# Performance work log

Measured on AMD Instinct MI355X. Metric: run time of the kernel, lower is better.

## Reference

```python
import jax, jax.numpy as jnp
import numpy as np

S_INDEX, E_INDEX = 3, 5
S = 26
C = 80
IMG_SIZE = 416.0
LAMBDA_COORD = 5.0
LAMBDA_NOOBJ = 0.5
YOLO_STEP = 3
N = YOLO_STEP * (5 + C)  # 255
ANCHOR = jnp.array([[10, 13], [16, 30], [33, 23], [30, 61], [62, 45],
                    [59, 119], [116, 90], [156, 198], [373, 326]], dtype=jnp.float32)
B, NB = 256, 32


def setup_inputs() -> dict:
    key = jax.random.key(0)
    k1, k2, k3, k4, k5 = jax.random.split(key, 5)
    batch_x = jax.random.normal(k1, (B, N, S, S), dtype=jnp.float32)
    cls = jax.random.randint(k2, (B, NB), 0, C).astype(jnp.float32)
    cxy = jax.random.uniform(k3, (B, NB, 2), minval=0.0, maxval=IMG_SIZE - 1e-3)
    wh = jax.random.uniform(k4, (B, NB, 2), minval=5.0, maxval=IMG_SIZE / 2)
    batch_box = jnp.concatenate([cls[..., None], cxy, wh], axis=-1)  # [B, NB, 5]
    batch_index = jax.random.randint(k5, (B, NB), S_INDEX, E_INDEX + 1)  # anchors of this scale
    return {"batch_x": batch_x, "batch_box": batch_box, "batch_index": batch_index}


def _iou(b1, b2):
    # torch IOU with +1 area convention and negative values clipped to 0
    A = (b1[:, 2] - b1[:, 0] + 1) * (b1[:, 3] - b1[:, 1] + 1)
    Bt = (b2[:, 2] - b2[:, 0] + 1) * (b2[:, 3] - b2[:, 1] + 1)
    CM = ((jnp.minimum(b1[:, 2], b2[:, 2]) - jnp.maximum(b1[:, 0], b2[:, 0]) + 1) *
          (jnp.minimum(b1[:, 3], b2[:, 3]) - jnp.maximum(b1[:, 1], b2[:, 1]) + 1))
    r = CM / (A + Bt - CM)
    return jnp.where(r < 0, 0.0, r)


def _image_loss(x, box, n_index):
    # x: [N, S, S], box: [nb, 5] = (class, cx, cy, w, h), n_index: [nb] global anchor ids
    nb = box.shape[0]
    div = IMG_SIZE / S
    now_index = n_index - S_INDEX            # local anchor id in {0,1,2}
    base = now_index * (5 + C)               # channel offset per box
    ix = (box[:, 1] / div).astype(jnp.int32)
    iy = (box[:, 2] / div).astype(jnp.int32)
    ax = (box[:, 1] - ix.astype(x.dtype) * div) / div
    ay = (box[:, 2] - iy.astype(x.dtype) * div) / div
    now_x = x[:, ix, iy]                     # [N, nb] gather of responsible cells
    it = jnp.arange(nb)
    obj_pred = now_x[base, it]
    rax = now_x[base + 1, it]
    ray = now_x[base + 2, it]
    rw = ANCHOR[n_index, 0] * jnp.exp(4.0 * jax.nn.sigmoid(now_x[base + 3, it]) - 2.0)
    rh = ANCHOR[n_index, 1] * jnp.exp(4.0 * jax.nn.sigmoid(now_x[base + 4, it]) - 2.0)
    b1 = jnp.stack([rax * div - rw / 2, ray * div - rh / 2,
                    rax * div + rw / 2, ray * div + rh / 2], axis=1)
    b2 = jnp.stack([ax * div - box[:, 3] / 2, ay * div - box[:, 4] / 2,
                    ax * div + box[:, 3] / 2, ay * div + box[:, 4] / 2], axis=1)
    iou = _iou(b1, b2)
    hot = jax.nn.one_hot(box[:, 0].astype(jnp.int32), C, dtype=x.dtype)
    lbl_idx = base[:, None] + 5 + jnp.arange(C)[None, :]   # [nb, C]
    label = now_x[lbl_idx, it[:, None]]                     # [nb, C]
    mse = lambda a, b: jnp.mean((a - b) ** 2)
    loss = LAMBDA_COORD * mse(obj_pred, iou)
    loss = loss + mse(label, hot)
    loss = loss + LAMBDA_COORD * mse(rax, ax)
    loss = loss + LAMBDA_COORD * mse(ray, ay)
    loss = loss + LAMBDA_COORD * mse(rw / IMG_SIZE, box[:, 3] / IMG_SIZE)
    loss = loss + LAMBDA_COORD * mse(rh / IMG_SIZE, box[:, 4] / IMG_SIZE)
    # no-object loss over the 3 objectness channels, minus responsible cells
    mask = jnp.zeros((N, S, S), dtype=bool)
    mask = mask.at[jnp.array([0, 5 + C, 2 * (5 + C)])].set(True)
    mask = mask.at[base, ix, iy].set(False)
    cnt = jnp.sum(mask).astype(x.dtype)
    noobj = jnp.sum(jnp.where(mask, x, 0.0) ** 2) / cnt
    return loss + LAMBDA_NOOBJ * noobj


def reference(batch_x, batch_box, batch_index):
    losses = jax.vmap(_image_loss)(batch_x, batch_box, batch_index)  # [B]
    return jnp.sum(losses).reshape(1)
```

## Files before the change

### kernel.cpp

```cpp
#include <hip/hip_runtime.h>

#define S_DIM 26
#define NCLS 80
#define CELLS 676
#define NB 32
#define NCH 255
#define NPLANE 2028
#define CH_BLK 85

__global__ __launch_bounds__(256)
void yolo_loss_kernel(const float* __restrict__ x,
                      const float* __restrict__ box,
                      const int*   __restrict__ nidx,
                      float* __restrict__ out)
{
    const int b   = blockIdx.x;
    const int tid = threadIdx.x;
    const float* xb = x + (size_t)b * (NCH * CELLS);

    __shared__ int   s_key[NB];
    __shared__ int   s_off[NB];
    __shared__ int   s_cls[NB];
    __shared__ float s_obj2[NB];
    __shared__ float s_part[4][4];

    float accA = 0.f;
    float accL = 0.f;
    float accP = 0.f;
    float accD = 0.f;
    float accC = 0.f;

    if (tid < NB) {
        const float* bx = box + ((size_t)b * NB + tid) * 5;
        float cls = bx[0], cx = bx[1], cy = bx[2], w = bx[3], h = bx[4];
        int n  = nidx[b * NB + tid];
        int ni = n - 3;
        int ix = (int)(cx * (1.0f / 16.0f));
        int iy = (int)(cy * (1.0f / 16.0f));
        float ax = (cx - (float)ix * 16.0f) * (1.0f / 16.0f);
        float ay = (cy - (float)iy * 16.0f) * (1.0f / 16.0f);
        int cell = ix * S_DIM + iy;
        int off  = ni * CH_BLK * CELLS + cell;

        s_key[tid] = ni * CELLS + cell;
        s_off[tid] = off;
        s_cls[tid] = (int)cls;

        float obj = xb[off];
        float rax = xb[off + 1 * CELLS];
        float ray = xb[off + 2 * CELLS];
        float t3  = xb[off + 3 * CELLS];
        float t4  = xb[off + 4 * CELLS];
        s_obj2[tid] = obj * obj;

        const float AW[3] = {30.f, 62.f, 59.f};
        const float AH[3] = {61.f, 45.f, 119.f};
        float sig3 = 1.0f / (1.0f + expf(-t3));
        float sig4 = 1.0f / (1.0f + expf(-t4));
        float rw = AW[ni] * expf(4.0f * sig3 - 2.0f);
        float rh = AH[ni] * expf(4.0f * sig4 - 2.0f);

        float b1x0 = rax * 16.f - rw * 0.5f, b1y0 = ray * 16.f - rh * 0.5f;
        float b1x1 = rax * 16.f + rw * 0.5f, b1y1 = ray * 16.f + rh * 0.5f;
        float b2x0 = ax * 16.f - w * 0.5f,   b2y0 = ay * 16.f - h * 0.5f;
        float b2x1 = ax * 16.f + w * 0.5f,   b2y1 = ay * 16.f + h * 0.5f;
        float A  = (rw + 1.f) * (rh + 1.f);
        float Bt = (w + 1.f) * (h + 1.f);
        float CM = (fminf(b1x1, b2x1) - fmaxf(b1x0, b2x0) + 1.f) *
                   (fminf(b1y1, b2y1) - fmaxf(b1y0, b2y0) + 1.f);
        float r = CM / (A + Bt - CM);
        float iou = (r < 0.f) ? 0.f : r;

        float d;
        d = obj - iou;                  accA += d * d;
        d = rax - ax;                   accA += d * d;
        d = ray - ay;                   accA += d * d;
        d = (rw - w) * (1.f / 416.f);   accA += d * d;
        d = (rh - h) * (1.f / 416.f);   accA += d * d;
    }
    __syncthreads();

    if (tid < NB) {
        int key = s_key[tid];
        bool first = true;
        for (int s = 0; s < tid; ++s)
            if (s_key[s] == key) { first = false; break; }
        if (first) { accC += 1.0f; accD += s_obj2[tid]; }
    }

    for (int u = tid; u < NB * NCLS; u += 256) {
        int t = u / NCLS;
        int c = u - t * NCLS;
        float val = xb[s_off[t] + (5 + c) * CELLS];
        float hot = (c == s_cls[t]) ? 1.0f : 0.0f;
        float d = val - hot;
        accL += d * d;
    }

    for (int u = tid; u < NPLANE; u += 256) {
        int pl   = u / CELLS;
        int cell = u - pl * CELLS;
        float v = xb[pl * CH_BLK * CELLS + cell];
        accP += v * v;
    }

    float v1 = accA * (5.0f / 32.0f) + accL * (1.0f / 2560.0f);
    float v2 = accP;
    float v3 = accD;
    float v4 = accC;
    #pragma unroll
    for (int o = 32; o > 0; o >>= 1) {
        v1 += __shfl_down(v1, o, 64);
        v2 += __shfl_down(v2, o, 64);
        v3 += __shfl_down(v3, o, 64);
        v4 += __shfl_down(v4, o, 64);
    }
    int wave = tid >> 6;
    if ((tid & 63) == 0) {
        s_part[0][wave] = v1; s_part[1][wave] = v2;
        s_part[2][wave] = v3; s_part[3][wave] = v4;
    }
    __syncthreads();
    if (tid == 0) {
        float t1 = s_part[0][0] + s_part[0][1] + s_part[0][2] + s_part[0][3];
        float t2 = s_part[1][0] + s_part[1][1] + s_part[1][2] + s_part[1][3];
        float t3 = s_part[2][0] + s_part[2][1] + s_part[2][2] + s_part[2][3];
        float t4 = s_part[3][0] + s_part[3][1] + s_part[3][2] + s_part[3][3];
        float cnt  = 2028.0f - t4;
        float loss = t1 + 0.5f * (t2 - t3) / cnt;
        atomicAdd(out, loss);
    }
}

extern "C" void kernel_launch(void* const* d_in, const int* in_sizes, int n_in,
                              void* d_out, int out_size, void* d_ws, size_t ws_size,
                              hipStream_t stream) {
    const float* x    = (const float*)d_in[0];
    const float* box  = (const float*)d_in[1];
    const int*   nidx = (const int*)d_in[2];
    float* out = (float*)d_out;

    hipMemsetAsync(out, 0, sizeof(float) * out_size, stream);
    yolo_loss_kernel<<<dim3(256), dim3(256), 0, stream>>>(x, box, nidx, out);
}
```

Before: 228.0 us.

## Split per-image loss across three blocks and vectorize objectness plane reads

Launches three blocks per image instead of one. One block sums squared values over the three objectness planes using float4 loads. The other two each handle 16 boxes' head and class terms, and each contributes its partial loss through an atomicAdd. The aim is more parallelism across the GPU and fewer serialized loads per block. The cost is three times as many atomics, repeated metadata setup, and an unused unscaled kernel variant left in the file.

```diff
diff --git a/kernel.cpp b/kernel.cpp
--- a/kernel.cpp
+++ b/kernel.cpp
@@ -5,8 +5,47 @@
 #define CELLS 676
 #define NB 32
 #define NCH 255
-#define NPLANE 2028
 #define CH_BLK 85
+#define PLANE_F4 507
+#define F4_PER_PLANE 169
+#define F4_PLANE_STRIDE 14365
+
+__device__ inline float head_terms(const float* __restrict__ xb,
+                                   int off, int ni,
+                                   float w, float h, float ax, float ay)
+{
+    float obj = xb[off];
+    float rax = xb[off + 1 * CELLS];
+    float ray = xb[off + 2 * CELLS];
+    float t3  = xb[off + 3 * CELLS];
+    float t4  = xb[off + 4 * CELLS];
+
+    const float AW[3] = {30.f, 62.f, 59.f};
+    const float AH[3] = {61.f, 45.f, 119.f};
+    float sig3 = 1.0f / (1.0f + expf(-t3));
+    float sig4 = 1.0f / (1.0f + expf(-t4));
+    float rw = AW[ni] * expf(4.0f * sig3 - 2.0f);
+    float rh = AH[ni] * expf(4.0f * sig4 - 2.0f);
+
+    float b1x0 = rax * 16.f - rw * 0.5f, b1y0 = ray * 16.f - rh * 0.5f;
+    float b1x1 = rax * 16.f + rw * 0.5f, b1y1 = ray * 16.f + rh * 0.5f;
+    float b2x0 = ax * 16.f - w * 0.5f,   b2y0 = ay * 16.f - h * 0.5f;
+    float b2x1 = ax * 16.f + w * 0.5f,   b2y1 = ay * 16.f + h * 0.5f;
+    float A  = (rw + 1.f) * (rh + 1.f);
+    float Bt = (w + 1.f) * (h + 1.f);
+    float CM = (fminf(b1x1, b2x1) - fmaxf(b1x0, b2x0) + 1.f) *
+               (fminf(b1y1, b2y1) - fmaxf(b1y0, b2y0) + 1.f);
+    float r = CM / (A + Bt - CM);
+    float iou = (r < 0.f) ? 0.f : r;
+
+    float acc = 0.f, d;
+    d = obj - iou;                  acc += d * d;
+    d = rax - ax;                   acc += d * d;
+    d = ray - ay;                   acc += d * d;
+    d = (rw - w) * (1.f / 416.f);   acc += d * d;
+    d = (rh - h) * (1.f / 416.f);   acc += d * d;
+    return acc;
+}
 
 __global__ __launch_bounds__(256)
 void yolo_loss_kernel(const float* __restrict__ x,
@@ -14,121 +53,217 @@
                       const int*   __restrict__ nidx,
                       float* __restrict__ out)
 {
-    const int b   = blockIdx.x;
-    const int tid = threadIdx.x;
+    const int b     = blockIdx.x;
+    const int slice = blockIdx.y;
+    const int tid   = threadIdx.x;
     const float* xb = x + (size_t)b * (NCH * CELLS);
 
     __shared__ int   s_key[NB];
     __shared__ int   s_off[NB];
     __shared__ int   s_cls[NB];
     __shared__ float s_obj2[NB];
-    __shared__ float s_part[4][4];
-
-    float accA = 0.f;
-    float accL = 0.f;
-    float accP = 0.f;
-    float accD = 0.f;
-    float accC = 0.f;
-
-    if (tid < NB) {
-        const float* bx = box + ((size_t)b * NB + tid) * 5;
-        float cls = bx[0], cx = bx[1], cy = bx[2], w = bx[3], h = bx[4];
-        int n  = nidx[b * NB + tid];
-        int ni = n - 3;
-        int ix = (int)(cx * (1.0f / 16.0f));
-        int iy = (int)(cy * (1.0f / 16.0f));
-        float ax = (cx - (float)ix * 16.0f) * (1.0f / 16.0f);
-        float ay = (cy - (float)iy * 16.0f) * (1.0f / 16.0f);
-        int cell = ix * S_DIM + iy;
-        int off  = ni * CH_BLK * CELLS + cell;
-
-        s_key[tid] = ni * CELLS + cell;
-        s_off[tid] = off;
-        s_cls[tid] = (int)cls;
-
-        float obj = xb[off];
-        float rax = xb[off + 1 * CELLS];
-        float ray = xb[off + 2 * CELLS];
-        float t3  = xb[off + 3 * CELLS];
-        float t4  = xb[off + 4 * CELLS];
-        s_obj2[tid] = obj * obj;
-
-        const float AW[3] = {30.f, 62.f, 59.f};
-        const float AH[3] = {61.f, 45.f, 119.f};
-        float sig3 = 1.0f / (1.0f + expf(-t3));
-        float sig4 = 1.0f / (1.0f + expf(-t4));
-        float rw = AW[ni] * expf(4.0f * sig3 - 2.0f);
-        float rh = AH[ni] * expf(4.0f * sig4 - 2.0f);
-
-        float b1x0 = rax * 16.f - rw * 0.5f, b1y0 = ray * 16.f - rh * 0.5f;
-        float b1x1 = rax * 16.f + rw * 0.5f, b1y1 = ray * 16.f + rh * 0.5f;
-        float b2x0 = ax * 16.f - w * 0.5f,   b2y0 = ay * 16.f - h * 0.5f;
-        float b2x1 = ax * 16.f + w * 0.5f,   b2y1 = ay * 16.f + h * 0.5f;
-        float A  = (rw + 1.f) * (rh + 1.f);
-        float Bt = (w + 1.f) * (h + 1.f);
-        float CM = (fminf(b1x1, b2x1) - fmaxf(b1x0, b2x0) + 1.f) *
-                   (fminf(b1y1, b2y1) - fmaxf(b1y0, b2y0) + 1.f);
-        float r = CM / (A + Bt - CM);
-        float iou = (r < 0.f) ? 0.f : r;
-
-        float d;
-        d = obj - iou;                  accA += d * d;
-        d = rax - ax;                   accA += d * d;
-        d = ray - ay;                   accA += d * d;
-        d = (rw - w) * (1.f / 416.f);   accA += d * d;
-        d = (rh - h) * (1.f / 416.f);   accA += d * d;
-    }
-    __syncthreads();
-
-    if (tid < NB) {
-        int key = s_key[tid];
-        bool first = true;
-        for (int s = 0; s < tid; ++s)
-            if (s_key[s] == key) { first = false; break; }
-        if (first) { accC += 1.0f; accD += s_obj2[tid]; }
-    }
-
-    for (int u = tid; u < NB * NCLS; u += 256) {
-        int t = u / NCLS;
-        int c = u - t * NCLS;
-        float val = xb[s_off[t] + (5 + c) * CELLS];
-        float hot = (c == s_cls[t]) ? 1.0f : 0.0f;
-        float d = val - hot;
-        accL += d * d;
-    }
-
-    for (int u = tid; u < NPLANE; u += 256) {
-        int pl   = u / CELLS;
-        int cell = u - pl * CELLS;
-        float v = xb[pl * CH_BLK * CELLS + cell];
-        accP += v * v;
-    }
-
-    float v1 = accA * (5.0f / 32.0f) + accL * (1.0f / 2560.0f);
-    float v2 = accP;
-    float v3 = accD;
-    float v4 = accC;
+    __shared__ float s_red[3][4];
+
+    float r0 = 0.f, r1 = 0.f, r2 = 0.f;
+
+    if (slice == 2) {
+        if (tid < NB) {
+            const float* bx = box + ((size_t)b * NB + tid) * 5;
+            float cx = bx[1], cy = bx[2];
+            int ni = nidx[b * NB + tid] - 3;
+            int ix = (int)(cx * 0.0625f);
+            int iy = (int)(cy * 0.0625f);
+            s_key[tid] = ni * CELLS + ix * S_DIM + iy;
+        }
+        __syncthreads();
+        if (tid < NB) {
+            bool first = true;
+            for (int s = 0; s < tid; ++s)
+                if (s_key[s] == s_key[tid]) { first = false; break; }
+            if (first) r1 += 1.0f;
+        }
+        const float4* p4 = (const float4*)xb;
+        #pragma unroll
+        for (int u = tid; u < PLANE_F4; u += 256) {
+            int pl = (u >= 2 * F4_PER_PLANE) ? 2 : (u >= F4_PER_PLANE ? 1 : 0);
+            int i4 = u - pl * F4_PER_PLANE;
+            float4 v = p4[pl * F4_PLANE_STRIDE + i4];
+            r0 += v.x * v.x + v.y * v.y + v.z * v.z + v.w * v.w;
+        }
+    } else {
+        const int boxbase = slice * 16;
+        const int nboxes_meta = (slice == 0) ? NB : 16;
+        if (tid < nboxes_meta) {
+            int gbox = (slice == 0) ? tid : (boxbase + tid);
+            const float* bx = box + ((size_t)b * NB + gbox) * 5;
+            float cls = bx[0], cx = bx[1], cy = bx[2], w = bx[3], h = bx[4];
+            int ni = nidx[b * NB + gbox] - 3;
+            int ix = (int)(cx * 0.0625f);
+            int iy = (int)(cy * 0.0625f);
+            float ax = (cx - (float)ix * 16.0f) * 0.0625f;
+            float ay = (cy - (float)iy * 16.0f) * 0.0625f;
+            int cell = ix * S_DIM + iy;
+            int off  = ni * CH_BLK * CELLS + cell;
+            s_key[tid] = ni * CELLS + cell;
+            s_off[tid] = off;
+            s_cls[tid] = (int)cls;
+            if (slice == 0) s_obj2[tid] = xb[off] * xb[off];
+            if (tid < 16)
+                r0 += head_terms(xb, off, ni, w, h, ax, ay);
+        }
+        __syncthreads();
+        if (slice == 0 && tid < NB) {
+            bool first = true;
+            for (int s = 0; s < tid; ++s)
+                if (s_key[s] == s_key[tid]) { first = false; break; }
+            if (first) { r2 += 1.0f; r1 += s_obj2[tid]; }
+        }
+        #pragma unroll
+        for (int u = tid; u < 16 * NCLS; u += 256) {
+            int t = u / NCLS;
+            int c = u - t * NCLS;
+            int lt = (slice == 0) ? t : t;
+            float val = xb[s_off[lt] + (5 + c) * CELLS];
+            float hot = (c == s_cls[lt]) ? 1.0f : 0.0f;
+            float d = val - hot;
+            r0 += d * d;
+        }
+    }
+
+
     #pragma unroll
     for (int o = 32; o > 0; o >>= 1) {
-        v1 += __shfl_down(v1, o, 64);
-        v2 += __shfl_down(v2, o, 64);
-        v3 += __shfl_down(v3, o, 64);
-        v4 += __shfl_down(v4, o, 64);
+        r0 += __shfl_down(r0, o, 64);
+        r1 += __shfl_down(r1, o, 64);
+        r2 += __shfl_down(r2, o, 64);
     }
     int wave = tid >> 6;
-    if ((tid & 63) == 0) {
-        s_part[0][wave] = v1; s_part[1][wave] = v2;
-        s_part[2][wave] = v3; s_part[3][wave] = v4;
-    }
+    if ((tid & 63) == 0) { s_red[0][wave] = r0; s_red[1][wave] = r1; s_red[2][wave] = r2; }
     __syncthreads();
     if (tid == 0) {
-        float t1 = s_part[0][0] + s_part[0][1] + s_part[0][2] + s_part[0][3];
-        float t2 = s_part[1][0] + s_part[1][1] + s_part[1][2] + s_part[1][3];
-        float t3 = s_part[2][0] + s_part[2][1] + s_part[2][2] + s_part[2][3];
-        float t4 = s_part[3][0] + s_part[3][1] + s_part[3][2] + s_part[3][3];
-        float cnt  = 2028.0f - t4;
-        float loss = t1 + 0.5f * (t2 - t3) / cnt;
-        atomicAdd(out, loss);
+        float t0 = s_red[0][0] + s_red[0][1] + s_red[0][2] + s_red[0][3];
+        float t1 = s_red[1][0] + s_red[1][1] + s_red[1][2] + s_red[1][3];
+        float t2 = s_red[2][0] + s_red[2][1] + s_red[2][2] + s_red[2][3];
+        float contrib;
+        if (slice == 2) {
+            float cnt = 2028.0f - t1;
+            contrib = 0.5f * t0 / cnt;
+        } else if (slice == 0) {
+            float cnt = 2028.0f - t2;
+            contrib = t0 - 0.5f * t1 / cnt;
+        } else {
+            contrib = t0;
+        }
+        atomicAdd(out, contrib);
+    }
+}
+
+
+__global__ __launch_bounds__(256)
+void yolo_loss_kernel_scaled(const float* __restrict__ x,
+                             const float* __restrict__ box,
+                             const int*   __restrict__ nidx,
+                             float* __restrict__ out)
+{
+    const int b     = blockIdx.x;
+    const int slice = blockIdx.y;
+    const int tid   = threadIdx.x;
+    const float* xb = x + (size_t)b * (NCH * CELLS);
+
+    __shared__ int   s_key[NB];
+    __shared__ int   s_off[NB];
+    __shared__ int   s_cls[NB];
+    __shared__ float s_obj2[NB];
+    __shared__ float s_red[3][4];
+
+    float r0 = 0.f, r1 = 0.f, r2 = 0.f;
+
+    if (slice == 2) {
+        if (tid < NB) {
+            const float* bx = box + ((size_t)b * NB + tid) * 5;
+            float cx = bx[1], cy = bx[2];
+            int ni = nidx[b * NB + tid] - 3;
+            int ix = (int)(cx * 0.0625f);
+            int iy = (int)(cy * 0.0625f);
+            s_key[tid] = ni * CELLS + ix * S_DIM + iy;
+        }
+        __syncthreads();
+        if (tid < NB) {
+            bool first = true;
+            for (int s = 0; s < tid; ++s)
+                if (s_key[s] == s_key[tid]) { first = false; break; }
+            if (first) r1 += 1.0f;
+        }
+        const float4* p4 = (const float4*)xb;
+        for (int u = tid; u < PLANE_F4; u += 256) {
+            int pl = (u >= 2 * F4_PER_PLANE) ? 2 : (u >= F4_PER_PLANE ? 1 : 0);
+            int i4 = u - pl * F4_PER_PLANE;
+            float4 v = p4[pl * F4_PLANE_STRIDE + i4];
+            r0 += v.x * v.x + v.y * v.y + v.z * v.z + v.w * v.w;
+        }
+    } else {
+        const int boxbase = slice * 16;
+        const int nmeta = (slice == 0) ? NB : 16;
+        if (tid < nmeta) {
+            int gbox = (slice == 0) ? tid : (boxbase + tid);
+            const float* bx = box + ((size_t)b * NB + gbox) * 5;
+            float cls = bx[0], cx = bx[1], cy = bx[2], w = bx[3], h = bx[4];
+            int ni = nidx[b * NB + gbox] - 3;
+            int ix = (int)(cx * 0.0625f);
+            int iy = (int)(cy * 0.0625f);
+            float ax = (cx - (float)ix * 16.0f) * 0.0625f;
+            float ay = (cy - (float)iy * 16.0f) * 0.0625f;
+            int cell = ix * S_DIM + iy;
+            int off  = ni * CH_BLK * CELLS + cell;
+            s_key[tid] = ni * CELLS + cell;
+            s_off[tid] = off;
+            s_cls[tid] = (int)cls;
+            if (slice == 0) s_obj2[tid] = xb[off] * xb[off];
+            bool do_head = (slice == 0) ? (tid < 16) : true;
+            if (do_head)
+                r0 += head_terms(xb, off, ni, w, h, ax, ay) * (5.0f / 32.0f);
+        }
+        __syncthreads();
+        if (slice == 0 && tid < NB) {
+            bool first = true;
+            for (int s = 0; s < tid; ++s)
+                if (s_key[s] == s_key[tid]) { first = false; break; }
+            if (first) { r2 += 1.0f; r1 += s_obj2[tid]; }
+        }
+        for (int u = tid; u < 16 * NCLS; u += 256) {
+            int t = u / NCLS;
+            int c = u - t * NCLS;
+            float val = xb[s_off[t] + (5 + c) * CELLS];
+            float hot = (c == s_cls[t]) ? 1.0f : 0.0f;
+            float d = val - hot;
+            r0 += d * d * (1.0f / 2560.0f);
+        }
+    }
+
+    #pragma unroll
+    for (int o = 32; o > 0; o >>= 1) {
+        r0 += __shfl_down(r0, o, 64);
+        r1 += __shfl_down(r1, o, 64);
+        r2 += __shfl_down(r2, o, 64);
+    }
+    int wave = tid >> 6;
+    if ((tid & 63) == 0) { s_red[0][wave] = r0; s_red[1][wave] = r1; s_red[2][wave] = r2; }
+    __syncthreads();
+    if (tid == 0) {
+        float t0 = s_red[0][0] + s_red[0][1] + s_red[0][2] + s_red[0][3];
+        float t1 = s_red[1][0] + s_red[1][1] + s_red[1][2] + s_red[1][3];
+        float t2 = s_red[2][0] + s_red[2][1] + s_red[2][2] + s_red[2][3];
+        float contrib;
+        if (slice == 2) {
+            float cnt = 2028.0f - t1;
+            contrib = 0.5f * t0 / cnt;
+        } else if (slice == 0) {
+            float cnt = 2028.0f - t2;
+            contrib = t0 - 0.5f * t1 / cnt;
+        } else {
+            contrib = t0;
+        }
+        atomicAdd(out, contrib);
     }
 }
 
@@ -141,5 +276,5 @@
     float* out = (float*)d_out;
 
     hipMemsetAsync(out, 0, sizeof(float) * out_size, stream);
-    yolo_loss_kernel<<<dim3(256), dim3(256), 0, stream>>>(x, box, nidx, out);
-}
+    yolo_loss_kernel_scaled<<<dim3(256, 3), dim3(256), 0, stream>>>(x, box, nidx, out);
+}
```

After: 226.7 us. Within noise of the previous version (-0.6%).
